# Kernel tuning notes

Hardware: AMD Instinct MI355X
Metric: run time of the kernel (lower is better)

Reference implementation:

```python
import jax, jax.numpy as jnp
import numpy as np

B, S, D, H, DH, BS, L, R, V, FF = 4, 4096, 768, 12, 64, 64, 2, 3, 50257, 3072
NB = S // BS          # 64 key/query blocks
NSEL = 5 + R          # 2 global + 3 window + R random key blocks per query block


def layer_norm(x, g, b, eps=1e-12):
    m = jnp.mean(x, axis=-1, keepdims=True)
    v = jnp.mean(jnp.square(x - m), axis=-1, keepdims=True)
    return (x - m) * jax.lax.rsqrt(v + eps) * g + b


def setup_inputs() -> dict:
    key = jax.random.key(0)
    ks = iter(jax.random.split(key, 16))
    p = lambda shape: jax.random.normal(next(ks), shape, jnp.float32) * 0.02
    return {
        'input_ids': jax.random.randint(next(ks), (B, S), 0, V, jnp.int32),
        'attention_mask': jnp.ones((B, S), jnp.int32),
        'label': jax.random.randint(next(ks), (B,), 0, 2, jnp.int32),
        'rand_idx': jax.random.randint(next(ks), (NB, R), 0, NB, jnp.int32),
        'emb': p((V, D)), 'pos_emb': p((S, D)),
        'ln_emb_g': jnp.ones((D,)), 'ln_emb_b': jnp.zeros((D,)),
        'Wqkv': p((L, D, 3 * D)), 'bqkv': jnp.zeros((L, 3 * D)),
        'Wo': p((L, D, D)), 'bo': jnp.zeros((L, D)),
        'ln1_g': jnp.ones((L, D)), 'ln1_b': jnp.zeros((L, D)),
        'Wff1': p((L, D, FF)), 'bff1': jnp.zeros((L, FF)),
        'Wff2': p((L, FF, D)), 'bff2': jnp.zeros((L, D)),
        'ln2_g': jnp.ones((L, D)), 'ln2_b': jnp.zeros((L, D)),
        'Wp': p((D, D)), 'bp': jnp.zeros((D,)),
        'Wc': p((D, 2)), 'bc': jnp.zeros((2,)),
    }


def reference(input_ids, attention_mask, label, rand_idx, emb, pos_emb,
              ln_emb_g, ln_emb_b, Wqkv, bqkv, Wo, bo, ln1_g, ln1_b,
              Wff1, bff1, Wff2, bff2, ln2_g, ln2_b, Wp, bp, Wc, bc):
    blk = jnp.arange(NB, dtype=jnp.int32)
    sel = jnp.concatenate([
        jnp.zeros((NB, 1), jnp.int32),
        ((blk - 1) % NB)[:, None], blk[:, None], ((blk + 1) % NB)[:, None],
        jnp.full((NB, 1), NB - 1, jnp.int32),
        rand_idx.astype(jnp.int32),
    ], axis=1)  # [NB, NSEL]

    h = emb[input_ids] + pos_emb[None]                 # [B,S,D]
    h = layer_norm(h, ln_emb_g, ln_emb_b)

    mblk = attention_mask.reshape(B, NB, BS)
    mask_sel = mblk[:, sel].reshape(B, 1, NB, 1, NSEL * BS)  # gathered key mask
    bias = jnp.where(mask_sel > 0, 0.0, -1e9).astype(h.dtype)

    scale = 1.0 / np.sqrt(DH)
    for l in range(L):
        qkv = h @ Wqkv[l] + bqkv[l]
        q, k, v = jnp.split(qkv, 3, axis=-1)
        to_blocks = lambda t: t.reshape(B, NB, BS, H, DH).transpose(0, 3, 1, 2, 4)  # [B,H,NB,BS,DH]
        qb, kb, vb = to_blocks(q), to_blocks(k), to_blocks(v)
        ksel = kb[:, :, sel].reshape(B, H, NB, NSEL * BS, DH)  # gather sparse key blocks
        vsel = vb[:, :, sel].reshape(B, H, NB, NSEL * BS, DH)
        scores = jnp.einsum('bhnqd,bhnkd->bhnqk', qb, ksel) * scale + bias
        attn = jax.nn.softmax(scores, axis=-1)
        ob = jnp.einsum('bhnqk,bhnkd->bhnqd', attn, vsel)
        o = ob.transpose(0, 2, 3, 1, 4).reshape(B, S, D)
        h = layer_norm(h + o @ Wo[l] + bo[l], ln1_g[l], ln1_b[l])
        ff = jax.nn.gelu(h @ Wff1[l] + bff1[l]) @ Wff2[l] + bff2[l]
        h = layer_norm(h + ff, ln2_g[l], ln2_b[l])

    pooled = jnp.tanh(h[:, 0] @ Wp + bp)               # BERT-style pooler on [CLS]
    probs = jax.nn.softmax(pooled @ Wc + bc, axis=1)
    # Faithful to the original: CrossEntropyLoss applied to softmax OUTPUT (double softmax)
    loss = -jnp.mean(jax.nn.log_softmax(probs, axis=1)[jnp.arange(B), label])
    return probs, loss
```

## Files before the change

kernel.cpp:

```cpp
#include <hip/hip_runtime.h>
#include <hip/hip_bf16.h>
#include <stdint.h>


using bf16 = __hip_bfloat16;
typedef __bf16 bf16x8 __attribute__((ext_vector_type(8)));
typedef __bf16 bf16x4 __attribute__((ext_vector_type(4)));
typedef float f32x4 __attribute__((ext_vector_type(4)));

__device__ __forceinline__ float b2f(bf16 x) { return __bfloat162float(x); }
__device__ __forceinline__ bf16 f2b(float x) { return __float2bfloat16(x); }
__device__ __forceinline__ __bf16 f2br(float x) {
  bf16 h = __float2bfloat16(x);
  return *reinterpret_cast<__bf16*>(&h);
}
__device__ __forceinline__ float br2f(__bf16 x) {
  bf16 t; *reinterpret_cast<__bf16*>(&t) = x; return __bfloat162float(t);
}
__device__ __forceinline__ float ldf(const void* p, size_t i, int flag) {
  return flag ? __bfloat162float(((const bf16*)p)[i]) : ((const float*)p)[i];
}

__device__ __forceinline__ void gld_lds16(const bf16* g, bf16* l) {
  __builtin_amdgcn_global_load_lds((__attribute__((address_space(1))) void*)g,
                                   (__attribute__((address_space(3))) void*)l, 16, 0, 0);
}

__device__ __forceinline__ f32x4 mfma16(bf16x8 a, bf16x8 b, f32x4 c) {
  return __builtin_amdgcn_mfma_f32_16x16x32_bf16(a, b, c, 0, 0, 0);
}

__device__ __forceinline__ float gelu_f(float x) {
  const float z = 1.5957691216057308f * (x + 0.044715f * x * x * x);
  return x / (1.0f + __expf(-z));
}

__global__ void probe_kernel(const uint32_t* __restrict__ g, int* __restrict__ flag) {
  if (threadIdx.x == 0) flag[0] = (g[0] == 0x3F803F80u) ? 1 : 0;
}

__global__ __launch_bounds__(256) void transpose_k(const void* __restrict__ in, size_t in_off,
                                                   bf16* __restrict__ out, int K, int N,
                                                   const int* __restrict__ dflag) {
  __shared__ float tile[32][33];
  const int flag = dflag[0];
  const int bx = blockIdx.x * 32;
  const int by = blockIdx.y * 32;
  const int tx = threadIdx.x & 31, ty = threadIdx.x >> 5;
#pragma unroll
  for (int i = 0; i < 32; i += 8)
    tile[ty + i][tx] = ldf(in, in_off + (size_t)(by + ty + i) * N + bx + tx, flag);
  __syncthreads();
#pragma unroll
  for (int i = 0; i < 32; i += 8)
    out[(size_t)(bx + ty + i) * K + by + tx] = f2b(tile[tx][ty + i]);
}

__global__ __launch_bounds__(256) void embed_ln_kernel(
    const int* __restrict__ ids, const void* __restrict__ emb, const void* __restrict__ pos,
    const void* __restrict__ g, const void* __restrict__ bb, bf16* __restrict__ h,
    const int* __restrict__ dflag) {
  __shared__ float red[8];
  const int flag = dflag[0];
  const int tok = blockIdx.x;
  const int tid = threadIdx.x;
  const int s = tok & 4095;
  const size_t id = (size_t)ids[tok];
  float v[3]; float sum = 0.f, sq = 0.f;
#pragma unroll
  for (int i = 0; i < 3; i++) {
    const int d = tid + i * 256;
    v[i] = ldf(emb, id * 768 + d, flag) + ldf(pos, (size_t)s * 768 + d, flag);
    sum += v[i]; sq += v[i] * v[i];
  }
#pragma unroll
  for (int off = 32; off >= 1; off >>= 1) { sum += __shfl_down(sum, off); sq += __shfl_down(sq, off); }
  if ((tid & 63) == 0) { red[(tid >> 6) * 2] = sum; red[(tid >> 6) * 2 + 1] = sq; }
  __syncthreads();
  sum = red[0] + red[2] + red[4] + red[6];
  sq  = red[1] + red[3] + red[5] + red[7];
  const float mean = sum * (1.0f / 768.0f);
  const float var = sq * (1.0f / 768.0f) - mean * mean;
  const float rs = rsqrtf(var + 1e-12f);
  bf16* hr = h + (size_t)tok * 768;
#pragma unroll
  for (int i = 0; i < 3; i++) {
    const int d = tid + i * 256;
    hr[d] = f2b((v[i] - mean) * rs * ldf(g, d, flag) + ldf(bb, d, flag));
  }
}

__global__ __launch_bounds__(256) void add_ln_kernel(
    bf16* __restrict__ h, const bf16* __restrict__ x,
    const void* __restrict__ g, const void* __restrict__ bb, size_t goff,
    const int* __restrict__ dflag) {
  const int flag = dflag[0];
  const int tid = threadIdx.x;
  const int wv = tid >> 6, lane = tid & 63;
  const int tok = blockIdx.x * 4 + wv;
  const size_t base = (size_t)tok * 768;

  float v[16];
  float sum = 0.f, sq = 0.f;
  const bf16x8 h0 = *(const bf16x8*)(h + base + lane * 8);
  const bf16x8 x0 = *(const bf16x8*)(x + base + lane * 8);
#pragma unroll
  for (int j = 0; j < 8; j++) {
    const float t = br2f(h0[j]) + br2f(x0[j]);
    v[j] = t; sum += t; sq += t * t;
  }
  if (lane < 32) {
    const bf16x8 h1 = *(const bf16x8*)(h + base + 512 + lane * 8);
    const bf16x8 x1 = *(const bf16x8*)(x + base + 512 + lane * 8);
#pragma unroll
    for (int j = 0; j < 8; j++) {
      const float t = br2f(h1[j]) + br2f(x1[j]);
      v[8 + j] = t; sum += t; sq += t * t;
    }
  }
#pragma unroll
  for (int off = 32; off >= 1; off >>= 1) { sum += __shfl_xor(sum, off); sq += __shfl_xor(sq, off); }
  const float mean = sum * (1.0f / 768.0f);
  const float var = sq * (1.0f / 768.0f) - mean * mean;
  const float rs = rsqrtf(var + 1e-12f);

  bf16x8 o0;
#pragma unroll
  for (int j = 0; j < 8; j++) {
    const int d = lane * 8 + j;
    o0[j] = f2br((v[j] - mean) * rs * ldf(g, goff + d, flag) + ldf(bb, goff + d, flag));
  }
  *(bf16x8*)(h + base + lane * 8) = o0;
  if (lane < 32) {
    bf16x8 o1;
#pragma unroll
    for (int j = 0; j < 8; j++) {
      const int d = 512 + lane * 8 + j;
      o1[j] = f2br((v[8 + j] - mean) * rs * ldf(g, goff + d, flag) + ldf(bb, goff + d, flag));
    }
    *(bf16x8*)(h + base + 512 + lane * 8) = o1;
  }
}

template <int EPI, bool ABLK>
__global__ __launch_bounds__(256) void gemm_bt(
    const bf16* __restrict__ A, const bf16* __restrict__ Bt,
    const void* __restrict__ bias, size_t bias_off, bf16* __restrict__ C,
    int N, int K,
    bf16* __restrict__ qout, bf16* __restrict__ kout, bf16* __restrict__ vout,
    const int* __restrict__ dflag) {
  __shared__ __align__(16) bf16 smem[24576];
  const int m0 = blockIdx.x * 128;
  const int n0 = blockIdx.y * 128;
  const int tid = threadIdx.x;
  const int lane = tid & 63;
  const int wv = tid >> 6;
  const int wm = wv >> 1, wn = wv & 1;
  const int col = lane & 15, quad = lane >> 4;

  f32x4 acc[4][4] = {};

  const int sr = tid >> 2;
  const int kc = ((tid & 3) - ((tid >> 4) & 3)) & 3;
  const int sc = kc * 8;
  const bf16* gA = A + (size_t)(m0 + sr) * K + sc;
  const bf16* gB = Bt + (size_t)(n0 + sr) * K + sc;
  const size_t rstep = (size_t)64 * K;

  size_t cb0 = 0, cb1 = 0;
  if constexpr (ABLK) {
    const int t0 = m0 + sr, t1 = t0 + 64;
    cb0 = (size_t)(t0 >> 12) * 3145728 + ((t0 >> 6) & 63) * 4096 + (t0 & 63) * 64;
    cb1 = (size_t)(t1 >> 12) * 3145728 + ((t1 >> 6) & 63) * 4096 + (t1 & 63) * 64;
  }

  const int sl = (quad + (col >> 2)) & 3;

  auto stage = [&](int buf, int kk) {
    bf16* dA = smem + buf * 8192;
    bf16* dB = dA + 4096;
    const bf16 *pA0, *pA1;
    if constexpr (ABLK) {
      const int c = kk + sc;
      const int hh = c >> 6, dh = c & 63;
      pA0 = A + cb0 + hh * 262144 + dh;
      pA1 = A + cb1 + hh * 262144 + dh;
    } else {
      pA0 = gA + kk; pA1 = gA + rstep + kk;
    }
    gld_lds16(pA0, dA + tid * 8);
    gld_lds16(pA1, dA + 2048 + tid * 8);
    gld_lds16(gB + kk, dB + tid * 8);
    gld_lds16(gB + rstep + kk, dB + 2048 + tid * 8);
  };

  const int nIter = K >> 5;
  stage(0, 0);
  stage(1, 32);

  int cur = 0, pf = 2;
  for (int it = 0; it < nIter; ++it) {
    if (it + 2 < nIter) {
      stage(pf, (it + 2) * 32);
      pf = (pf == 2) ? 0 : pf + 1;
      asm volatile("s_waitcnt vmcnt(8)" ::: "memory");
    } else if (it + 1 < nIter) {
      asm volatile("s_waitcnt vmcnt(4)" ::: "memory");
    } else {
      asm volatile("s_waitcnt vmcnt(0)" ::: "memory");
    }
    __builtin_amdgcn_s_barrier();
    asm volatile("" ::: "memory");

    const bf16* cA = smem + cur * 8192;
    const bf16* cB = cA + 4096;
    bf16x8 av[4], bv[4];
#pragma unroll
    for (int t = 0; t < 4; t++)
      av[t] = *(const bf16x8*)(cA + (wm * 64 + t * 16 + col) * 32 + sl * 8);
#pragma unroll
    for (int t = 0; t < 4; t++)
      bv[t] = *(const bf16x8*)(cB + (wn * 64 + t * 16 + col) * 32 + sl * 8);
#pragma unroll
    for (int mt = 0; mt < 4; mt++)
#pragma unroll
      for (int nt = 0; nt < 4; nt++)
        acc[mt][nt] = mfma16(av[mt], bv[nt], acc[mt][nt]);

    asm volatile("" ::: "memory");
    __builtin_amdgcn_s_barrier();
    cur = (cur == 2) ? 0 : cur + 1;
  }

  const int flag = dflag[0];
  float bsv[4];
#pragma unroll
  for (int nt = 0; nt < 4; nt++)
    bsv[nt] = ldf(bias, bias_off + n0 + wn * 64 + nt * 16 + col, flag);

  if constexpr (EPI != 2) {
#pragma unroll
    for (int nt = 0; nt < 4; nt++)
#pragma unroll
      for (int mt = 0; mt < 4; mt++)
#pragma unroll
        for (int r = 0; r < 4; r++) {
          float val = acc[mt][nt][r] + bsv[nt];
          if constexpr (EPI == 1) val = gelu_f(val);
          smem[(wm * 64 + mt * 16 + quad * 4 + r) * 136 + wn * 64 + nt * 16 + col] = f2b(val);
        }
    __syncthreads();
#pragma unroll
    for (int rr = 0; rr < 8; rr++) {
      const int row = rr * 16 + (tid >> 4);
      const int ch = tid & 15;
      const bf16x8 vv = *(const bf16x8*)(smem + row * 136 + ch * 8);
      *(bf16x8*)(C + (size_t)(m0 + row) * N + n0 + ch * 8) = vv;
    }
  } else {
    const int part = (n0 >= 1536) ? 2 : ((n0 >= 768) ? 1 : 0);
    const int w0 = n0 - part * 768;
    const int h0 = w0 >> 6;
    const int bb = m0 >> 12;
    for (int half = 0; half < 2; half++) {
      const int nb_ = ((m0 >> 6) & 63) + half;
      __syncthreads();
      if (wm == half) {
        if (part < 2) {
#pragma unroll
          for (int nt = 0; nt < 4; nt++)
#pragma unroll
            for (int mt = 0; mt < 4; mt++)
#pragma unroll
              for (int r = 0; r < 4; r++)
                smem[(mt * 16 + quad * 4 + r) * 136 + wn * 64 + nt * 16 + col] =
                    f2b(acc[mt][nt][r] + bsv[nt]);
        } else {
#pragma unroll
          for (int nt = 0; nt < 4; nt++) {
            const int ncol = wn * 64 + nt * 16 + col;
#pragma unroll
            for (int mt = 0; mt < 4; mt++) {
              bf16x4 pk;
#pragma unroll
              for (int r = 0; r < 4; r++) pk[r] = f2br(acc[mt][nt][r] + bsv[nt]);
              *(bf16x4*)(smem + ncol * 72 + mt * 16 + quad * 4) = pk;
            }
          }
        }
      }
      __syncthreads();
      const int j = tid >> 7;
      const size_t dbase = (size_t)((bb * 12 + h0 + j) * 64 + nb_) * 4096;
      if (part < 2) {
        bf16* dst = (part == 0) ? qout : kout;
#pragma unroll
        for (int rr = 0; rr < 4; rr++) {
          const int tsk = (tid & 127) + rr * 128;
          const int row = tsk >> 3, pc = tsk & 7;
          const bf16x8 vv = *(const bf16x8*)(smem + row * 136 + j * 64 + pc * 8);
          *(bf16x8*)(dst + dbase + row * 64 + pc * 8) = vv;
        }
      } else {
#pragma unroll
        for (int rr = 0; rr < 4; rr++) {
          const int tsk = (tid & 127) + rr * 128;
          const int dh = tsk >> 3, pc = tsk & 7;
          const bf16x8 vv = *(const bf16x8*)(smem + (j * 64 + dh) * 72 + pc * 8);
          *(bf16x8*)(vout + dbase + dh * 64 + pc * 8) = vv;
        }
      }
    }
  }
}

__global__ __launch_bounds__(256, 4) void attn_kernel(
    const bf16* q, const bf16* __restrict__ kmat, const bf16* __restrict__ vT,
    const int* __restrict__ amask, const int* __restrict__ rand_idx, bf16* o) {
  __shared__ __align__(16) bf16 sK[2][4096];
  __shared__ __align__(16) bf16 sV[2][4096];
  const int idx = blockIdx.x;
  const int nb = idx & 63;
  const int bh = idx >> 6;
  const int bb = bh / 12;
  const int tid = threadIdx.x;
  const int wv = tid >> 6, lane = tid & 63;
  const int col = lane & 15, quad = lane >> 4;

  int sel[8];
  sel[0] = 0; sel[1] = (nb + 63) & 63; sel[2] = nb; sel[3] = (nb + 1) & 63;
  sel[4] = 63;
  sel[5] = rand_idx[nb * 3 + 0];
  sel[6] = rand_idx[nb * 3 + 1];
  sel[7] = rand_idx[nb * 3 + 2];

  const size_t bhbase = (size_t)bh * 64;

  const bf16* qb = q + (bhbase + nb) * 4096;
  const int qrow = wv * 16 + col;
  const bf16x8 bq0 = *(const bf16x8*)(qb + qrow * 64 + quad * 8);
  const bf16x8 bq1 = *(const bf16x8*)(qb + qrow * 64 + 32 + quad * 8);

  unsigned long long bal[8];
#pragma unroll
  for (int sb = 0; sb < 8; sb++)
    bal[sb] = __ballot(amask[bb * 4096 + sel[sb] * 64 + lane] > 0);

  const int srow = tid >> 3, sslot = tid & 7;
  const int sw0 = ((sslot ^ (srow & 7)) << 3);

  auto stage = [&](int buf, int blk) {
    const bf16* gk = kmat + (bhbase + blk) * 4096;
    const bf16* gv = vT + (bhbase + blk) * 4096;
    bf16* dk = sK[buf];
    bf16* dv = sV[buf];
    gld_lds16(gk + srow * 64 + sw0, dk + tid * 8);
    gld_lds16(gk + (srow + 32) * 64 + sw0, dk + 2048 + tid * 8);
    gld_lds16(gv + srow * 64 + sw0, dv + tid * 8);
    gld_lds16(gv + (srow + 32) * 64 + sw0, dv + 2048 + tid * 8);
  };

  f32x4 oacc[4] = {};
  float mrun = -1e30f, lrun = 0.0f;

  stage(0, sel[0]);

#pragma unroll
  for (int sb = 0; sb < 8; sb++) {
    const int cur = sb & 1;
    if (sb < 7) {
      stage(cur ^ 1, sel[sb + 1]);
      asm volatile("s_waitcnt vmcnt(4)" ::: "memory");
    } else {
      asm volatile("s_waitcnt vmcnt(0)" ::: "memory");
    }
    __builtin_amdgcn_s_barrier();
    asm volatile("" ::: "memory");

    const bf16* kb = sK[cur];
    f32x4 t[4];
#pragma unroll
    for (int c = 0; c < 4; c++) {
      const int r = c * 16 + col;
      const bf16x8 ak0 = *(const bf16x8*)(kb + r * 64 + ((quad ^ (r & 7)) << 3));
      const bf16x8 ak1 = *(const bf16x8*)(kb + r * 64 + (((4 + quad) ^ (r & 7)) << 3));
      f32x4 s4 = {};
      s4 = mfma16(ak0, bq0, s4);
      s4 = mfma16(ak1, bq1, s4);
      t[c] = s4;
    }
#pragma unroll
    for (int c = 0; c < 4; c++)
#pragma unroll
      for (int r = 0; r < 4; r++) t[c][r] *= 0.125f;
    if (bal[sb] != ~0ull) {
#pragma unroll
      for (int c = 0; c < 4; c++)
#pragma unroll
        for (int r = 0; r < 4; r++)
          if (!((bal[sb] >> (c * 16 + quad * 4 + r)) & 1)) t[c][r] -= 1e9f;
    }

    float pm = t[0][0];
#pragma unroll
    for (int c = 0; c < 4; c++)
#pragma unroll
      for (int r = 0; r < 4; r++) pm = fmaxf(pm, t[c][r]);
    pm = fmaxf(pm, __shfl_xor(pm, 16));
    pm = fmaxf(pm, __shfl_xor(pm, 32));

    const float mnew = fmaxf(mrun, pm);
    const float scale = __expf(mrun - mnew);
    float ps = 0.0f;
    bf16x8 pa8[2];
#pragma unroll
    for (int c = 0; c < 4; c++)
#pragma unroll
      for (int r = 0; r < 4; r++) {
        const float p = __expf(t[c][r] - mnew);
        ps += p;
        pa8[c >> 1][(c & 1) * 4 + r] = f2br(p);
      }
    ps += __shfl_xor(ps, 16);
    ps += __shfl_xor(ps, 32);
    lrun = lrun * scale + ps;
    mrun = mnew;

    float sc[4];
#pragma unroll
    for (int r = 0; r < 4; r++) sc[r] = __shfl(scale, quad * 4 + r);
#pragma unroll
    for (int nt = 0; nt < 4; nt++)
#pragma unroll
      for (int r = 0; r < 4; r++) oacc[nt][r] *= sc[r];

    const bf16* vb = sV[cur];
#pragma unroll
    for (int pr = 0; pr < 2; pr++) {
      const int g0 = 4 * pr + (quad >> 1);
      const int g1 = g0 + 2;
      const int so = (quad & 1) * 4;
#pragma unroll
      for (int nt = 0; nt < 4; nt++) {
        const int dh = nt * 16 + col;
        const bf16x4 bv0 = *(const bf16x4*)(vb + dh * 64 + ((g0 ^ (col & 7)) << 3) + so);
        const bf16x4 bv1 = *(const bf16x4*)(vb + dh * 64 + ((g1 ^ (col & 7)) << 3) + so);
        const bf16x8 bv8 = __builtin_shufflevector(bv0, bv1, 0, 1, 2, 3, 4, 5, 6, 7);
        oacc[nt] = mfma16(pa8[pr], bv8, oacc[nt]);
      }
    }
    asm volatile("" ::: "memory");
    __builtin_amdgcn_s_barrier();
  }

  const float invl = 1.0f / lrun;
  float iv[4];
#pragma unroll
  for (int r = 0; r < 4; r++) iv[r] = __shfl(invl, quad * 4 + r);
  bf16* ob = o + (bhbase + nb) * 4096;
#pragma unroll
  for (int nt = 0; nt < 4; nt++)
#pragma unroll
    for (int r = 0; r < 4; r++)
      ob[(wv * 16 + quad * 4 + r) * 64 + nt * 16 + col] = f2b(oacc[nt][r] * iv[r]);
}

__global__ __launch_bounds__(768) void pooler_kernel(
    const bf16* __restrict__ h, const void* __restrict__ Wp,
    const void* __restrict__ bp, float* __restrict__ pooled,
    const int* __restrict__ dflag) {
  __shared__ float hrow[768];
  const int flag = dflag[0];
  const int bb = blockIdx.x;
  const int j = threadIdx.x;
  hrow[j] = b2f(h[(size_t)bb * 4096 * 768 + j]);
  __syncthreads();
  float acc = 0.0f;
#pragma unroll 8
  for (int d = 0; d < 768; d++) acc += hrow[d] * ldf(Wp, (size_t)d * 768 + j, flag);
  pooled[bb * 768 + j] = tanhf(acc + ldf(bp, j, flag));
}

__global__ __launch_bounds__(256) void cls_kernel(
    const float* __restrict__ pooled, const void* __restrict__ Wc, const void* __restrict__ bc,
    const int* __restrict__ label, void* __restrict__ out, const int* __restrict__ dflag) {
  __shared__ float lsum[8];
  const int flag = dflag[0];
  const int tid = threadIdx.x;
  const int p = tid >> 5, i = tid & 31;
  const int bb = p >> 1, c = p & 1;
  float acc = 0.0f;
  for (int d = i; d < 768; d += 32) acc += pooled[bb * 768 + d] * ldf(Wc, (size_t)d * 2 + c, flag);
#pragma unroll
  for (int off = 16; off >= 1; off >>= 1) acc += __shfl_xor(acc, off);
  if (i == 0) lsum[p] = acc;
  __syncthreads();
  if (tid == 0) {
    float res[9];
    float loss = 0.0f;
    for (int b = 0; b < 4; b++) {
      const float l0 = lsum[b * 2 + 0] + ldf(bc, 0, flag);
      const float l1 = lsum[b * 2 + 1] + ldf(bc, 1, flag);
      const float m = fmaxf(l0, l1);
      const float e0 = expf(l0 - m), e1 = expf(l1 - m);
      const float s = e0 + e1;
      const float p0 = e0 / s, p1 = e1 / s;
      res[b * 2] = p0; res[b * 2 + 1] = p1;
      const float mm = fmaxf(p0, p1);
      const float lse = mm + logf(expf(p0 - mm) + expf(p1 - mm));
      const float chosen = (label[b] == 0) ? p0 : p1;
      loss -= (chosen - lse);
    }
    res[8] = loss * 0.25f;
    if (flag) { bf16* o = (bf16*)out; for (int j = 0; j < 9; j++) o[j] = f2b(res[j]); }
    else      { float* o = (float*)out; for (int j = 0; j < 9; j++) o[j] = res[j]; }
  }
}

extern "C" void kernel_launch(void* const* d_in, const int* in_sizes, int n_in,
                              void* d_out, int out_size, void* d_ws, size_t ws_size,
                              hipStream_t stream) {
  const int* input_ids      = (const int*)d_in[0];
  const int* attention_mask = (const int*)d_in[1];
  const int* label          = (const int*)d_in[2];
  const int* rand_idx       = (const int*)d_in[3];
  const void* emb      = d_in[4];
  const void* pos_emb  = d_in[5];
  const void* ln_emb_g = d_in[6];
  const void* ln_emb_b = d_in[7];
  const void* Wqkv = d_in[8];
  const void* bqkv = d_in[9];
  const void* Wo   = d_in[10];
  const void* bo   = d_in[11];
  const void* ln1_g = d_in[12];
  const void* ln1_b = d_in[13];
  const void* Wff1 = d_in[14];
  const void* bff1 = d_in[15];
  const void* Wff2 = d_in[16];
  const void* bff2 = d_in[17];
  const void* ln2_g = d_in[18];
  const void* ln2_b = d_in[19];
  const void* Wp = d_in[20];
  const void* bp = d_in[21];
  const void* Wc = d_in[22];
  const void* bc = d_in[23];

  bf16* ws = (bf16*)d_ws;
  size_t off = 0;
  int* dflag = (int*)(ws + off); off += 8;
  bf16* WqkvT = ws + off; off += (size_t)2 * 2304 * 768;
  bf16* WoT   = ws + off; off += (size_t)2 * 768 * 768;
  bf16* Wff1T = ws + off; off += (size_t)2 * 3072 * 768;
  bf16* Wff2T = ws + off; off += (size_t)2 * 768 * 3072;
  bf16* hbuf  = ws + off; off += (size_t)16384 * 768;
  bf16* qo    = ws + off; off += (size_t)16384 * 768;
  bf16* kbf   = ws + off; off += (size_t)16384 * 768;
  bf16* vbf   = ws + off; off += (size_t)16384 * 768;
  bf16* xbf   = ws + off; off += (size_t)16384 * 768;
  bf16* a1buf = ws + off; off += (size_t)16384 * 3072;
  float* pooled = (float*)(ws + off); off += 6144;

  dim3 blk(256);

  probe_kernel<<<1, 64, 0, stream>>>((const uint32_t*)ln_emb_g, dflag);

  for (int l = 0; l < 2; l++) {
    transpose_k<<<dim3(72, 24), blk, 0, stream>>>(Wqkv, (size_t)l * 768 * 2304, WqkvT + (size_t)l * 2304 * 768, 768, 2304, dflag);
    transpose_k<<<dim3(24, 24), blk, 0, stream>>>(Wo, (size_t)l * 768 * 768, WoT + (size_t)l * 768 * 768, 768, 768, dflag);
    transpose_k<<<dim3(96, 24), blk, 0, stream>>>(Wff1, (size_t)l * 768 * 3072, Wff1T + (size_t)l * 3072 * 768, 768, 3072, dflag);
    transpose_k<<<dim3(24, 96), blk, 0, stream>>>(Wff2, (size_t)l * 3072 * 768, Wff2T + (size_t)l * 768 * 3072, 3072, 768, dflag);
  }

  embed_ln_kernel<<<16384, blk, 0, stream>>>(input_ids, emb, pos_emb, ln_emb_g, ln_emb_b, hbuf, dflag);

  for (int l = 0; l < 2; l++) {
    gemm_bt<2, false><<<dim3(128, 18), blk, 0, stream>>>(hbuf, WqkvT + (size_t)l * 2304 * 768, bqkv, (size_t)l * 2304,
                                                         nullptr, 2304, 768, qo, kbf, vbf, dflag);
    attn_kernel<<<3072, blk, 0, stream>>>(qo, kbf, vbf, attention_mask, rand_idx, qo);
    gemm_bt<0, true><<<dim3(128, 6), blk, 0, stream>>>(qo, WoT + (size_t)l * 768 * 768, bo, (size_t)l * 768,
                                                       xbf, 768, 768, nullptr, nullptr, nullptr, dflag);
    add_ln_kernel<<<4096, blk, 0, stream>>>(hbuf, xbf, ln1_g, ln1_b, (size_t)l * 768, dflag);
    gemm_bt<1, false><<<dim3(128, 24), blk, 0, stream>>>(hbuf, Wff1T + (size_t)l * 3072 * 768, bff1, (size_t)l * 3072,
                                                         a1buf, 3072, 768, nullptr, nullptr, nullptr, dflag);
    gemm_bt<0, false><<<dim3(128, 6), blk, 0, stream>>>(a1buf, Wff2T + (size_t)l * 768 * 3072, bff2, (size_t)l * 768,
                                                        xbf, 768, 3072, nullptr, nullptr, nullptr, dflag);
    add_ln_kernel<<<4096, blk, 0, stream>>>(hbuf, xbf, ln2_g, ln2_b, (size_t)l * 768, dflag);
  }

  pooler_kernel<<<4, dim3(768), 0, stream>>>(hbuf, Wp, bp, pooled, dflag);
  cls_kernel<<<1, blk, 0, stream>>>(pooled, Wc, bc, label, d_out, dflag);

  (void)in_sizes; (void)n_in; (void)out_size; (void)ws_size;
}
```

Baseline: 1.522 ms.

## Add 256x256-tile 512-thread GEMM for QKV and FFN projections

Introduces a new GEMM kernel with 256x256 output tiles, 8 waves, a 64-wide K step, double-buffered direct-to-LDS loads with XOR swizzling, and s_setprio around the MFMA bursts. It replaces the 128x128 kernel for the QKV, FF1 and FF2 projections, and the QKV head-split epilogue moves into it. The aim is more operand reuse per byte loaded and less global traffic. The trade-off is fewer workgroups (192 for FF2, 576 for QKV), which can underfill 256 CUs, plus 128KB of LDS per block, which limits occupancy to one block per CU.

After: 1.644 ms. +8.0%, slower.

```diff
diff --git a/kernel.cpp b/kernel.cpp
--- a/kernel.cpp
+++ b/kernel.cpp
@@ -139,6 +139,174 @@
       o1[j] = f2br((v[8 + j] - mean) * rs * ldf(g, goff + d, flag) + ldf(bb, goff + d, flag));
     }
     *(bf16x8*)(h + base + 512 + lane * 8) = o1;
+  }
+}
+
+template <int EPI>
+__global__ __launch_bounds__(512) void gemm256(
+    const bf16* __restrict__ A, const bf16* __restrict__ Bt,
+    const void* __restrict__ bias, size_t bias_off, bf16* __restrict__ C,
+    int N, int K,
+    bf16* __restrict__ qout, bf16* __restrict__ kout, bf16* __restrict__ vout,
+    const int* __restrict__ dflag) {
+  __shared__ __align__(16) bf16 smem[65536];
+  const int m0 = blockIdx.x * 256;
+  const int n0 = blockIdx.y * 256;
+  const int tid = threadIdx.x;
+  const int lane = tid & 63;
+  const int wv = tid >> 6;
+  const int wm = wv >> 2, wn = wv & 3;
+  const int col = lane & 15, quad = lane >> 4;
+
+  f32x4 acc[8][4] = {};
+
+  const int rS = tid >> 3, slS = tid & 7;
+  const int swz = (slS ^ (rS & 7)) << 3;
+  const bf16* gA = A + (size_t)(m0 + rS) * K + swz;
+  const bf16* gB = Bt + (size_t)(n0 + rS) * K + swz;
+  const size_t rowstep = (size_t)64 * K;
+
+  auto stage = [&](int buf, int kt) {
+    bf16* dA = smem + buf * 32768;
+    bf16* dB = dA + 16384;
+    const int kk = kt * 64;
+#pragma unroll
+    for (int i = 0; i < 4; i++)
+      gld_lds16(gA + (size_t)i * rowstep + kk, dA + i * 4096 + tid * 8);
+#pragma unroll
+    for (int i = 0; i < 4; i++)
+      gld_lds16(gB + (size_t)i * rowstep + kk, dB + i * 4096 + tid * 8);
+  };
+
+  const int nkt = K >> 6;
+  stage(0, 0);
+
+  const int arow = wm * 128 + col;
+  const int brow = wn * 64 + col;
+  const int s7 = col & 7;
+
+  for (int it = 0; it < nkt; ++it) {
+    const int cur = it & 1;
+    if (it + 1 < nkt) {
+      stage(cur ^ 1, it + 1);
+      asm volatile("s_waitcnt vmcnt(8)" ::: "memory");
+    } else {
+      asm volatile("s_waitcnt vmcnt(0)" ::: "memory");
+    }
+    __builtin_amdgcn_s_barrier();
+    asm volatile("" ::: "memory");
+
+    const bf16* cA = smem + cur * 32768;
+    const bf16* cB = cA + 16384;
+#pragma unroll
+    for (int kh = 0; kh < 2; kh++) {
+      const int ksl = ((kh * 4 + quad) ^ s7) << 3;
+      bf16x8 bv[4];
+#pragma unroll
+      for (int n = 0; n < 4; n++)
+        bv[n] = *(const bf16x8*)(cB + (brow + n * 16) * 64 + ksl);
+#pragma unroll
+      for (int mh = 0; mh < 2; mh++) {
+        bf16x8 av[4];
+#pragma unroll
+        for (int m = 0; m < 4; m++)
+          av[m] = *(const bf16x8*)(cA + (arow + (mh * 4 + m) * 16) * 64 + ksl);
+        __builtin_amdgcn_s_setprio(1);
+#pragma unroll
+        for (int m = 0; m < 4; m++)
+#pragma unroll
+          for (int n = 0; n < 4; n++)
+            acc[mh * 4 + m][n] = mfma16(av[m], bv[n], acc[mh * 4 + m][n]);
+        __builtin_amdgcn_s_setprio(0);
+        asm volatile("" ::: "memory");
+        __builtin_amdgcn_s_barrier();
+      }
+    }
+  }
+
+  const int flag = dflag[0];
+  float bsv[4];
+#pragma unroll
+  for (int nt = 0; nt < 4; nt++)
+    bsv[nt] = ldf(bias, bias_off + n0 + wn * 64 + nt * 16 + col, flag);
+
+  if constexpr (EPI != 2) {
+    for (int P = 0; P < 4; P++) {
+      __syncthreads();
+      if (wm == (P >> 1)) {
+        const int mh = P & 1;
+#pragma unroll
+        for (int nt = 0; nt < 4; nt++)
+#pragma unroll
+          for (int m = 0; m < 4; m++)
+#pragma unroll
+            for (int r = 0; r < 4; r++) {
+              float val = acc[mh * 4 + m][nt][r] + bsv[nt];
+              if constexpr (EPI == 1) val = gelu_f(val);
+              smem[(m * 16 + quad * 4 + r) * 264 + wn * 64 + nt * 16 + col] = f2b(val);
+            }
+      }
+      __syncthreads();
+#pragma unroll
+      for (int j = 0; j < 4; j++) {
+        const int c2 = j * 512 + tid;
+        const int row = c2 >> 5, cc = c2 & 31;
+        const bf16x8 vv = *(const bf16x8*)(smem + row * 264 + cc * 8);
+        *(bf16x8*)(C + (size_t)(m0 + P * 64 + row) * N + n0 + cc * 8) = vv;
+      }
+    }
+  } else {
+    const int part = n0 / 768;
+    const int w0 = n0 - part * 768;
+    const int h0 = w0 >> 6;
+    const int bb = m0 >> 12;
+    const int nb0 = (m0 >> 6) & 63;
+    for (int P = 0; P < 4; P++) {
+      __syncthreads();
+      if (wm == (P >> 1)) {
+        const int mh = P & 1;
+        if (part < 2) {
+#pragma unroll
+          for (int nt = 0; nt < 4; nt++)
+#pragma unroll
+            for (int m = 0; m < 4; m++)
+#pragma unroll
+              for (int r = 0; r < 4; r++)
+                smem[(m * 16 + quad * 4 + r) * 264 + wn * 64 + nt * 16 + col] =
+                    f2b(acc[mh * 4 + m][nt][r] + bsv[nt]);
+        } else {
+#pragma unroll
+          for (int nt = 0; nt < 4; nt++) {
+            const int ncol = wn * 64 + nt * 16 + col;
+#pragma unroll
+            for (int m = 0; m < 4; m++) {
+              bf16x4 pk;
+#pragma unroll
+              for (int r = 0; r < 4; r++) pk[r] = f2br(acc[mh * 4 + m][nt][r] + bsv[nt]);
+              *(bf16x4*)(smem + ncol * 72 + m * 16 + quad * 4) = pk;
+            }
+          }
+        }
+      }
+      __syncthreads();
+      const size_t nbase = (size_t)((bb * 12 + h0) * 64 + nb0 + P) * 4096;
+      if (part < 2) {
+        bf16* dst = (part == 0) ? qout : kout;
+        const int pos = tid >> 3, pc = tid & 7;
+#pragma unroll
+        for (int j = 0; j < 4; j++) {
+          const bf16x8 vv = *(const bf16x8*)(smem + pos * 264 + j * 64 + pc * 8);
+          *(bf16x8*)(dst + nbase + (size_t)j * 262144 + pos * 64 + pc * 8) = vv;
+        }
+      } else {
+        const int dh = tid >> 3, pc = tid & 7;
+#pragma unroll
+        for (int j = 0; j < 4; j++) {
+          const bf16x8 vv = *(const bf16x8*)(smem + (j * 64 + dh) * 72 + pc * 8);
+          *(bf16x8*)(vout + nbase + (size_t)j * 262144 + dh * 64 + pc * 8) = vv;
+        }
+      }
+    }
   }
 }
 
@@ -238,80 +406,25 @@
   for (int nt = 0; nt < 4; nt++)
     bsv[nt] = ldf(bias, bias_off + n0 + wn * 64 + nt * 16 + col, flag);
 
-  if constexpr (EPI != 2) {
-#pragma unroll
-    for (int nt = 0; nt < 4; nt++)
-#pragma unroll
-      for (int mt = 0; mt < 4; mt++)
-#pragma unroll
-        for (int r = 0; r < 4; r++) {
-          float val = acc[mt][nt][r] + bsv[nt];
-          if constexpr (EPI == 1) val = gelu_f(val);
-          smem[(wm * 64 + mt * 16 + quad * 4 + r) * 136 + wn * 64 + nt * 16 + col] = f2b(val);
-        }
-    __syncthreads();
-#pragma unroll
-    for (int rr = 0; rr < 8; rr++) {
-      const int row = rr * 16 + (tid >> 4);
-      const int ch = tid & 15;
-      const bf16x8 vv = *(const bf16x8*)(smem + row * 136 + ch * 8);
-      *(bf16x8*)(C + (size_t)(m0 + row) * N + n0 + ch * 8) = vv;
-    }
-  } else {
-    const int part = (n0 >= 1536) ? 2 : ((n0 >= 768) ? 1 : 0);
-    const int w0 = n0 - part * 768;
-    const int h0 = w0 >> 6;
-    const int bb = m0 >> 12;
-    for (int half = 0; half < 2; half++) {
-      const int nb_ = ((m0 >> 6) & 63) + half;
-      __syncthreads();
-      if (wm == half) {
-        if (part < 2) {
-#pragma unroll
-          for (int nt = 0; nt < 4; nt++)
-#pragma unroll
-            for (int mt = 0; mt < 4; mt++)
-#pragma unroll
-              for (int r = 0; r < 4; r++)
-                smem[(mt * 16 + quad * 4 + r) * 136 + wn * 64 + nt * 16 + col] =
-                    f2b(acc[mt][nt][r] + bsv[nt]);
-        } else {
-#pragma unroll
-          for (int nt = 0; nt < 4; nt++) {
-            const int ncol = wn * 64 + nt * 16 + col;
-#pragma unroll
-            for (int mt = 0; mt < 4; mt++) {
-              bf16x4 pk;
-#pragma unroll
-              for (int r = 0; r < 4; r++) pk[r] = f2br(acc[mt][nt][r] + bsv[nt]);
-              *(bf16x4*)(smem + ncol * 72 + mt * 16 + quad * 4) = pk;
-            }
-          }
-        }
+#pragma unroll
+  for (int nt = 0; nt < 4; nt++)
+#pragma unroll
+    for (int mt = 0; mt < 4; mt++)
+#pragma unroll
+      for (int r = 0; r < 4; r++) {
+        float val = acc[mt][nt][r] + bsv[nt];
+        if constexpr (EPI == 1) val = gelu_f(val);
+        smem[(wm * 64 + mt * 16 + quad * 4 + r) * 136 + wn * 64 + nt * 16 + col] = f2b(val);
       }
-      __syncthreads();
-      const int j = tid >> 7;
-      const size_t dbase = (size_t)((bb * 12 + h0 + j) * 64 + nb_) * 4096;
-      if (part < 2) {
-        bf16* dst = (part == 0) ? qout : kout;
-#pragma unroll
-        for (int rr = 0; rr < 4; rr++) {
-          const int tsk = (tid & 127) + rr * 128;
-          const int row = tsk >> 3, pc = tsk & 7;
-          const bf16x8 vv = *(const bf16x8*)(smem + row * 136 + j * 64 + pc * 8);
-          *(bf16x8*)(dst + dbase + row * 64 + pc * 8) = vv;
-        }
-      } else {
-#pragma unroll
-        for (int rr = 0; rr < 4; rr++) {
-          const int tsk = (tid & 127) + rr * 128;
-          const int dh = tsk >> 3, pc = tsk & 7;
-          const bf16x8 vv = *(const bf16x8*)(smem + (j * 64 + dh) * 72 + pc * 8);
-          *(bf16x8*)(vout + dbase + dh * 64 + pc * 8) = vv;
-        }
-      }
-    }
-  }
+  __syncthreads();
+#pragma unroll
+  for (int rr = 0; rr < 8; rr++) {
+    const int row = rr * 16 + (tid >> 4);
+    const int ch = tid & 15;
+    const bf16x8 vv = *(const bf16x8*)(smem + row * 136 + ch * 8);
+    *(bf16x8*)(C + (size_t)(m0 + row) * N + n0 + ch * 8) = vv;
+  }
+  (void)qout; (void)kout; (void)vout;
 }
 
 __global__ __launch_bounds__(256, 4) void attn_kernel(
@@ -561,6 +674,7 @@
   float* pooled = (float*)(ws + off); off += 6144;
 
   dim3 blk(256);
+  dim3 blk512(512);
 
   probe_kernel<<<1, 64, 0, stream>>>((const uint32_t*)ln_emb_g, dflag);
 
@@ -574,16 +688,16 @@
   embed_ln_kernel<<<16384, blk, 0, stream>>>(input_ids, emb, pos_emb, ln_emb_g, ln_emb_b, hbuf, dflag);
 
   for (int l = 0; l < 2; l++) {
-    gemm_bt<2, false><<<dim3(128, 18), blk, 0, stream>>>(hbuf, WqkvT + (size_t)l * 2304 * 768, bqkv, (size_t)l * 2304,
-                                                         nullptr, 2304, 768, qo, kbf, vbf, dflag);
+    gemm256<2><<<dim3(64, 9), blk512, 0, stream>>>(hbuf, WqkvT + (size_t)l * 2304 * 768, bqkv, (size_t)l * 2304,
+                                                   nullptr, 2304, 768, qo, kbf, vbf, dflag);
     attn_kernel<<<3072, blk, 0, stream>>>(qo, kbf, vbf, attention_mask, rand_idx, qo);
     gemm_bt<0, true><<<dim3(128, 6), blk, 0, stream>>>(qo, WoT + (size_t)l * 768 * 768, bo, (size_t)l * 768,
                                                        xbf, 768, 768, nullptr, nullptr, nullptr, dflag);
     add_ln_kernel<<<4096, blk, 0, stream>>>(hbuf, xbf, ln1_g, ln1_b, (size_t)l * 768, dflag);
-    gemm_bt<1, false><<<dim3(128, 24), blk, 0, stream>>>(hbuf, Wff1T + (size_t)l * 3072 * 768, bff1, (size_t)l * 3072,
-                                                         a1buf, 3072, 768, nullptr, nullptr, nullptr, dflag);
-    gemm_bt<0, false><<<dim3(128, 6), blk, 0, stream>>>(a1buf, Wff2T + (size_t)l * 768 * 3072, bff2, (size_t)l * 768,
-                                                        xbf, 768, 3072, nullptr, nullptr, nullptr, dflag);
+    gemm256<1><<<dim3(64, 12), blk512, 0, stream>>>(hbuf, Wff1T + (size_t)l * 3072 * 768, bff1, (size_t)l * 3072,
+                                                    a1buf, 3072, 768, nullptr, nullptr, nullptr, dflag);
+    gemm256<0><<<dim3(64, 3), blk512, 0, stream>>>(a1buf, Wff2T + (size_t)l * 768 * 3072, bff2, (size_t)l * 768,
+                                                   xbf, 768, 3072, nullptr, nullptr, nullptr, dflag);
     add_ln_kernel<<<4096, blk, 0, stream>>>(hbuf, xbf, ln2_g, ln2_b, (size_t)l * 768, dflag);
   }
 
```
